# Kernel tuning notes

Hardware: AMD Instinct MI355X
Metric: run time of the kernel (lower is better)

The kernel has to match this reference:

```python
import jax, jax.numpy as jnp
import numpy as np


def setup_inputs() -> dict:
    key = jax.random.key(0)
    kx, ke = jax.random.split(key)
    N, T, D, M = 64, 400, 1024, 256
    x = jax.random.normal(kx, (N, T, D), dtype=jnp.float32)
    embedding = jax.random.normal(ke, (M, D), dtype=jnp.float32)
    return {"x": x, "embedding": embedding}


def reference(x, embedding):
    # x: (N, T, D); embedding (codebook): (M, D)
    M, D = embedding.shape
    # L2_distance: normalize codebook rows, distances to detached x
    emb_norm = embedding / (jnp.linalg.norm(embedding, axis=1, keepdims=True) + 1e-4)
    x_flat = jax.lax.stop_gradient(x).reshape(-1, D)  # (N*T, D)
    distances = (jnp.sum(emb_norm ** 2, axis=1)[None, :]
                 + jnp.sum(x_flat ** 2, axis=1, keepdims=True)
                 - 2.0 * (x_flat @ emb_norm.T))  # (N*T, M)
    indices = jnp.argmin(distances, axis=-1)  # (N*T,)
    encodings = jax.nn.one_hot(indices, M, dtype=jnp.float32)  # (N*T, M)
    quantized = embedding[indices].reshape(x.shape)  # gather from UNnormalized codebook

    # commitment loss (both sides detached in original -> constant)
    commitment_loss = jnp.mean(
        (jax.lax.stop_gradient(x) - jax.lax.stop_gradient(quantized)) ** 2)

    # straight-through + average with quantized
    quantized_st = x + jax.lax.stop_gradient(quantized - x)
    quantized_ = (quantized_st + quantized) / 2.0

    avg_probs = jnp.mean(encodings, axis=0)  # (M,)
    perplexity = jnp.exp(-jnp.sum(avg_probs * jnp.log(avg_probs + 1e-10)))
    return quantized_, commitment_loss, perplexity
```

## Files before the change

kernel.cpp:

```cpp
#include <hip/hip_runtime.h>
#include <cstdint>
#include <cstddef>


typedef __attribute__((ext_vector_type(8))) short short8;
typedef __attribute__((ext_vector_type(4))) float f32x4;

namespace {
constexpr int kNT = 25600;
constexpr int kD  = 1024;
constexpr int kM  = 256;
constexpr size_t kQElems = (size_t)kNT * kD;

constexpr int WS_IMG_H = 0;
constexpr int WS_IMG_L = 131072;
constexpr int WS_E2N   = 262144;
constexpr int WS_SCL   = WS_E2N + kM;
constexpr int WS_E2R   = WS_SCL + kM;
constexpr int WS_COM   = WS_E2R + kM;
constexpr int WS_HIST  = WS_COM + 4;
constexpr int WS_ZERO_BYTES = (WS_HIST + kM - WS_COM) * 4;
}

typedef __attribute__((address_space(3))) unsigned int        lds_u32;
typedef const __attribute__((address_space(1))) unsigned int  glb_u32;
typedef const __attribute__((address_space(3))) char          lds_chc;

__device__ __forceinline__ void gl2lds16(const void* g, void* l) {
  __builtin_amdgcn_global_load_lds((glb_u32*)g, (lds_u32*)l, 16, 0, 0);
}

template <int OFF>
__device__ __forceinline__ short8 ldsr(lds_chc* p) {
  short8 r;
  asm volatile("ds_read_b128 %0, %1 offset:%c2" : "=v"(r) : "v"(p), "i"(OFF));
  return r;
}

__global__ __launch_bounds__(256) void vq_normalize(const float* __restrict__ emb,
                                                    float* __restrict__ ws) {
  const int m = blockIdx.x;
  const int t = threadIdx.x;
  const float4 v = reinterpret_cast<const float4*>(emb + (size_t)m * kD)[t];
  float s = v.x * v.x + v.y * v.y + v.z * v.z + v.w * v.w;
#pragma unroll
  for (int mask = 32; mask >= 1; mask >>= 1) s += __shfl_xor(s, mask);
  __shared__ float red[4];
  if ((t & 63) == 0) red[t >> 6] = s;
  __syncthreads();
  const float tot = red[0] + red[1] + red[2] + red[3];
  const float sc  = sqrtf(tot) + 1e-4f;
  const float inv = 1.0f / sc;
  const float4 nv = make_float4(v.x * inv, v.y * inv, v.z * inv, v.w * inv);

  float s2 = nv.x * nv.x + nv.y * nv.y + nv.z * nv.z + nv.w * nv.w;
#pragma unroll
  for (int mask = 32; mask >= 1; mask >>= 1) s2 += __shfl_xor(s2, mask);
  __syncthreads();
  if ((t & 63) == 0) red[t >> 6] = s2;
  __syncthreads();
  if (t == 0) {
    ws[WS_E2N + m] = red[0] + red[1] + red[2] + red[3];
    ws[WS_SCL + m] = sc;
    ws[WS_E2R + m] = tot;
  }

  unsigned short* imgh = (unsigned short*)(ws + WS_IMG_H);
  unsigned short* imgl = (unsigned short*)(ws + WS_IMG_L);
  const int c  = t >> 3;
  const int g  = (t >> 1) & 3;
  const int sq = g ^ ((m >> 1) & 3);
  const int base = c * 8192 + m * 32 + sq * 8 + 4 * (t & 1);
  ushort4 hq, lq;
#pragma unroll
  for (int j = 0; j < 4; ++j) {
    const float fv = (&nv.x)[j];
    const unsigned int b = __float_as_uint(fv);
    const unsigned short hi = (unsigned short)(b >> 16);
    const float lof = fv - __uint_as_float(b & 0xFFFF0000u);
    const unsigned short lo = (unsigned short)(__float_as_uint(lof) >> 16);
    (&hq.x)[j] = hi; (&lq.x)[j] = lo;
  }
  *(ushort4*)(imgh + base) = hq;
  *(ushort4*)(imgl + base) = lq;
}


#define RD8(BSEL, G, H0, H1, H2, H3, L0, L1, L2, L3)                           \
  H0 = ldsr<(BSEL) * 32768 + ((G) * 4 + 0) * 1024>(lbase);                     \
  H1 = ldsr<(BSEL) * 32768 + ((G) * 4 + 1) * 1024>(lbase);                     \
  H2 = ldsr<(BSEL) * 32768 + ((G) * 4 + 2) * 1024>(lbase);                     \
  H3 = ldsr<(BSEL) * 32768 + ((G) * 4 + 3) * 1024>(lbase);                     \
  L0 = ldsr<(BSEL) * 32768 + 16384 + ((G) * 4 + 0) * 1024>(lbase);             \
  L1 = ldsr<(BSEL) * 32768 + 16384 + ((G) * 4 + 1) * 1024>(lbase);             \
  L2 = ldsr<(BSEL) * 32768 + 16384 + ((G) * 4 + 2) * 1024>(lbase);             \
  L3 = ldsr<(BSEL) * 32768 + 16384 + ((G) * 4 + 3) * 1024>(lbase);

#define MM12(G, H0, H1, H2, H3, L0, L1, L2, L3)                                              \
  acc[(G) * 4 + 0] = __builtin_amdgcn_mfma_f32_16x16x32_bf16(ah, H0, acc[(G) * 4 + 0], 0, 0, 0); \
  acc[(G) * 4 + 1] = __builtin_amdgcn_mfma_f32_16x16x32_bf16(ah, H1, acc[(G) * 4 + 1], 0, 0, 0); \
  acc[(G) * 4 + 2] = __builtin_amdgcn_mfma_f32_16x16x32_bf16(ah, H2, acc[(G) * 4 + 2], 0, 0, 0); \
  acc[(G) * 4 + 3] = __builtin_amdgcn_mfma_f32_16x16x32_bf16(ah, H3, acc[(G) * 4 + 3], 0, 0, 0); \
  acc[(G) * 4 + 0] = __builtin_amdgcn_mfma_f32_16x16x32_bf16(ah, L0, acc[(G) * 4 + 0], 0, 0, 0); \
  acc[(G) * 4 + 1] = __builtin_amdgcn_mfma_f32_16x16x32_bf16(ah, L1, acc[(G) * 4 + 1], 0, 0, 0); \
  acc[(G) * 4 + 2] = __builtin_amdgcn_mfma_f32_16x16x32_bf16(ah, L2, acc[(G) * 4 + 2], 0, 0, 0); \
  acc[(G) * 4 + 3] = __builtin_amdgcn_mfma_f32_16x16x32_bf16(ah, L3, acc[(G) * 4 + 3], 0, 0, 0); \
  acc[(G) * 4 + 0] = __builtin_amdgcn_mfma_f32_16x16x32_bf16(al, H0, acc[(G) * 4 + 0], 0, 0, 0); \
  acc[(G) * 4 + 1] = __builtin_amdgcn_mfma_f32_16x16x32_bf16(al, H1, acc[(G) * 4 + 1], 0, 0, 0); \
  acc[(G) * 4 + 2] = __builtin_amdgcn_mfma_f32_16x16x32_bf16(al, H2, acc[(G) * 4 + 2], 0, 0, 0); \
  acc[(G) * 4 + 3] = __builtin_amdgcn_mfma_f32_16x16x32_bf16(al, H3, acc[(G) * 4 + 3], 0, 0, 0);

#define VQ_ITER(KC, BSEL, XC0, XC1, XN0, XN1)                                  \
  {                                                                            \
    const int kcn_ = ((KC) < 31) ? (KC) + 1 : 31;                              \
    const float* xp_ = xrow + kcn_ * 32;                                       \
    XN0 = *(const float4*)xp_;                                                 \
    XN1 = *(const float4*)(xp_ + 4);                                           \
    {                                                                          \
      const unsigned short* sg_ = simg + ((size_t)kcn_ << 13) + soff;          \
      char* dg_ = &buf[(BSEL) ^ 1][0] + ldst;                                  \
      _Pragma("unroll")                                                        \
      for (int it_ = 0; it_ < 8; ++it_)                                        \
        gl2lds16(sg_ + it_ * 512, dg_ + it_ * 1024);                           \
    }                                                                          \
    asm volatile("s_waitcnt vmcnt(10)" ::: "memory");                          \
    __builtin_amdgcn_s_barrier();                                              \
    asm volatile("" ::: "memory");                                             \
    short8 ha0_, ha1_, ha2_, ha3_, la0_, la1_, la2_, la3_;                     \
    short8 hb0_, hb1_, hb2_, hb3_, lb0_, lb1_, lb2_, lb3_;                     \
    RD8((BSEL), 0, ha0_, ha1_, ha2_, ha3_, la0_, la1_, la2_, la3_)             \
    RD8((BSEL), 1, hb0_, hb1_, hb2_, hb3_, lb0_, lb1_, lb2_, lb3_)             \
    short8 ah, al;                                                             \
    {                                                                          \
      union { short8 v; unsigned short u[8]; } H_, L_;                         \
      const float fx_[8] = {XC0.x, XC0.y, XC0.z, XC0.w,                        \
                            XC1.x, XC1.y, XC1.z, XC1.w};                       \
      _Pragma("unroll")                                                        \
      for (int jj_ = 0; jj_ < 8; ++jj_) {                                      \
        const float fv_ = fx_[jj_];                                            \
        const unsigned int b_ = __float_as_uint(fv_);                          \
        H_.u[jj_] = (unsigned short)(b_ >> 16);                                \
        const float lo_ = fv_ - __uint_as_float(b_ & 0xFFFF0000u);             \
        L_.u[jj_] = (unsigned short)(__float_as_uint(lo_) >> 16);              \
        x2 += fv_ * fv_;                                                       \
      }                                                                        \
      ah = H_.v; al = L_.v;                                                    \
    }                                                                          \
    asm volatile("s_waitcnt lgkmcnt(8)" ::: "memory");                         \
    __builtin_amdgcn_sched_barrier(0);                                         \
    MM12(0, ha0_, ha1_, ha2_, ha3_, la0_, la1_, la2_, la3_)                    \
    RD8((BSEL), 2, ha0_, ha1_, ha2_, ha3_, la0_, la1_, la2_, la3_)             \
    asm volatile("s_waitcnt lgkmcnt(8)" ::: "memory");                         \
    __builtin_amdgcn_sched_barrier(0);                                         \
    MM12(1, hb0_, hb1_, hb2_, hb3_, lb0_, lb1_, lb2_, lb3_)                    \
    RD8((BSEL), 3, hb0_, hb1_, hb2_, hb3_, lb0_, lb1_, lb2_, lb3_)             \
    asm volatile("s_waitcnt lgkmcnt(8)" ::: "memory");                         \
    __builtin_amdgcn_sched_barrier(0);                                         \
    MM12(2, ha0_, ha1_, ha2_, ha3_, la0_, la1_, la2_, la3_)                    \
    asm volatile("s_waitcnt lgkmcnt(0)" ::: "memory");                         \
    __builtin_amdgcn_sched_barrier(0);                                         \
    MM12(3, hb0_, hb1_, hb2_, hb3_, lb0_, lb1_, lb2_, lb3_)                    \
    asm volatile("" ::: "memory");                                             \
    __builtin_amdgcn_s_barrier();                                              \
    asm volatile("" ::: "memory");                                             \
  }

__global__ __launch_bounds__(256, 2) void vq_main(const float* __restrict__ x,
                                                  const float* __restrict__ emb,
                                                  const float* __restrict__ wsc,
                                                  float* __restrict__ out,
                                                  float* __restrict__ commit_sum,
                                                  int* __restrict__ hist) {
  __shared__ char buf[2][32768];

  const int t   = threadIdx.x;
  const int l   = t & 63;
  const int w   = t >> 6;
  const int r0  = blockIdx.x * 64 + w * 16;
  const int nlo = l & 15;
  const int q   = l >> 4;
  const int sq  = q ^ ((l >> 1) & 3);

  const unsigned short* imgH = (const unsigned short*)(wsc + WS_IMG_H);
  const unsigned short* imgL = (const unsigned short*)(wsc + WS_IMG_L);
  const unsigned short* simg = (w & 2) ? imgL : imgH;
  const int soff = (w & 1) * 4096 + l * 8;
  const int ldst = w * 8192;

  const float* xrow = x + (size_t)(r0 + nlo) * kD + q * 8;
  lds_chc* lbase = (lds_chc*)&buf[0][0] + nlo * 64 + sq * 16;

  f32x4 acc[16];
#pragma unroll
  for (int i = 0; i < 16; ++i) acc[i] = (f32x4)0.0f;
  float x2 = 0.0f;

  float4 xa0, xa1, xb0, xb1;
  xa0 = *(const float4*)xrow;
  xa1 = *(const float4*)(xrow + 4);
  {
    const unsigned short* sg = simg + soff;
    char* dg = &buf[0][0] + ldst;
#pragma unroll
    for (int it = 0; it < 8; ++it) gl2lds16(sg + it * 512, dg + it * 1024);
  }

#pragma unroll 1
  for (int kk = 0; kk < 32; kk += 2) {
    VQ_ITER(kk,     0, xa0, xa1, xb0, xb1)
    VQ_ITER(kk + 1, 1, xb0, xb1, xa0, xa1)
  }

  x2 += __shfl_xor(x2, 16);
  x2 += __shfl_xor(x2, 32);

  float bv[4] = {3.0e38f, 3.0e38f, 3.0e38f, 3.0e38f};
  int   bj[4] = {0, 0, 0, 0};
#pragma unroll
  for (int ct = 0; ct < 16; ++ct) {
    const int j = ct * 16 + nlo;
    const float e = wsc[WS_E2N + j];
#pragma unroll
    for (int rg = 0; rg < 4; ++rg) {
      const float v = e - 2.0f * acc[ct][rg];
      if (v < bv[rg] || (v == bv[rg] && j < bj[rg])) { bv[rg] = v; bj[rg] = j; }
    }
  }
#pragma unroll
  for (int mk = 1; mk <= 8; mk <<= 1) {
#pragma unroll
    for (int rg = 0; rg < 4; ++rg) {
      const float ov = __shfl_xor(bv[rg], mk);
      const int   oj = __shfl_xor(bj[rg], mk);
      if (ov < bv[rg] || (ov == bv[rg] && oj < bj[rg])) { bv[rg] = ov; bj[rg] = oj; }
    }
  }

  float clq = 0.0f;
#pragma unroll
  for (int rg = 0; rg < 4; ++rg) {
    const int j = bj[rg];
    const float xr2 = __shfl(x2, (q << 2) | rg);
    clq += xr2 + wsc[WS_E2R + j] - (wsc[WS_E2N + j] - bv[rg]) * wsc[WS_SCL + j];
  }
  if (nlo == 0) {
#pragma unroll
    for (int rg = 0; rg < 4; ++rg) atomicAdd(&hist[bj[rg]], 1);
  }
  float cs = (nlo == 0) ? clq : 0.0f;
  cs += __shfl_xor(cs, 16);
  cs += __shfl_xor(cs, 32);
  if (l == 0) atomicAdd(commit_sum, cs);

  const float4* emb4 = (const float4*)emb;
  float4* out4 = (float4*)out;
#pragma unroll
  for (int r = 0; r < 16; ++r) {
    const int j = __shfl(bj[r & 3], (r >> 2) << 4);
    const float4* s = emb4 + (size_t)j * (kD / 4);
    float4* d = out4 + (size_t)(r0 + r) * (kD / 4);
#pragma unroll
    for (int c = 0; c < 4; ++c) d[c * 64 + l] = s[c * 64 + l];
  }
}

__global__ __launch_bounds__(256) void vq_final(const int* __restrict__ hist,
                                                const float* __restrict__ commit_sum,
                                                float* __restrict__ out) {
  const int t = threadIdx.x;
  const float p = (float)hist[t] * (1.0f / (float)kNT);
  float s = p * logf(p + 1e-10f);
#pragma unroll
  for (int mask = 32; mask >= 1; mask >>= 1) s += __shfl_xor(s, mask);
  __shared__ float red[4];
  if ((t & 63) == 0) red[t >> 6] = s;
  __syncthreads();
  if (t == 0) {
    const float ent = red[0] + red[1] + red[2] + red[3];
    out[kQElems]     = commit_sum[0] * (1.0f / (float)kQElems);
    out[kQElems + 1] = expf(-ent);
  }
}

extern "C" void kernel_launch(void* const* d_in, const int* in_sizes, int n_in,
                              void* d_out, int out_size, void* d_ws, size_t ws_size,
                              hipStream_t stream) {
  (void)in_sizes; (void)n_in; (void)out_size; (void)ws_size;
  const float* x   = (const float*)d_in[0];
  const float* emb = (const float*)d_in[1];
  float* out = (float*)d_out;
  float* ws  = (float*)d_ws;

  hipMemsetAsync((char*)d_ws + (size_t)WS_COM * 4, 0, WS_ZERO_BYTES, stream);
  hipLaunchKernelGGL(vq_normalize, dim3(kM), dim3(256), 0, stream, emb, ws);
  hipLaunchKernelGGL(vq_main, dim3(kNT / 64), dim3(256), 0, stream,
                     x, emb, ws, out, ws + WS_COM, (int*)(ws + WS_HIST));
  hipLaunchKernelGGL(vq_final, dim3(1), dim3(256), 0, stream,
                     (const int*)(ws + WS_HIST), ws + WS_COM, out);
}
```

Before: 252.6 us.

## Switch to 32x32x16 MFMA tiles with 128 rows per block

Replaces the 16x16x32 bf16 MFMA with 32x32x16 MFMA, so each wave now covers 32 rows instead of 16 and each block covers 128 rows. Every codebook tile staged in LDS is therefore reused across twice as many x rows, halving codebook traffic per row and the number of blocks. The argmin reduction and commitment-loss bookkeeping are reworked for the new accumulator layout, and the codebook norm arrays are cached in shared memory. In exchange, accumulator register use doubles, launch bounds drop to one block per CU, and there are only 200 blocks, which may underfill the GPU's CUs.

```diff
diff --git a/kernel.cpp b/kernel.cpp
--- a/kernel.cpp
+++ b/kernel.cpp
@@ -3,8 +3,8 @@
 #include <cstddef>
 
 
-typedef __attribute__((ext_vector_type(8))) short short8;
-typedef __attribute__((ext_vector_type(4))) float f32x4;
+typedef __attribute__((ext_vector_type(8)))  short short8;
+typedef __attribute__((ext_vector_type(16))) float f32x16;
 
 namespace {
 constexpr int kNT = 25600;
@@ -86,100 +86,110 @@
 }
 
 
-#define RD8(BSEL, G, H0, H1, H2, H3, L0, L1, L2, L3)                           \
-  H0 = ldsr<(BSEL) * 32768 + ((G) * 4 + 0) * 1024>(lbase);                     \
-  H1 = ldsr<(BSEL) * 32768 + ((G) * 4 + 1) * 1024>(lbase);                     \
-  H2 = ldsr<(BSEL) * 32768 + ((G) * 4 + 2) * 1024>(lbase);                     \
-  H3 = ldsr<(BSEL) * 32768 + ((G) * 4 + 3) * 1024>(lbase);                     \
-  L0 = ldsr<(BSEL) * 32768 + 16384 + ((G) * 4 + 0) * 1024>(lbase);             \
-  L1 = ldsr<(BSEL) * 32768 + 16384 + ((G) * 4 + 1) * 1024>(lbase);             \
-  L2 = ldsr<(BSEL) * 32768 + 16384 + ((G) * 4 + 2) * 1024>(lbase);             \
-  L3 = ldsr<(BSEL) * 32768 + 16384 + ((G) * 4 + 3) * 1024>(lbase);
-
-#define MM12(G, H0, H1, H2, H3, L0, L1, L2, L3)                                              \
-  acc[(G) * 4 + 0] = __builtin_amdgcn_mfma_f32_16x16x32_bf16(ah, H0, acc[(G) * 4 + 0], 0, 0, 0); \
-  acc[(G) * 4 + 1] = __builtin_amdgcn_mfma_f32_16x16x32_bf16(ah, H1, acc[(G) * 4 + 1], 0, 0, 0); \
-  acc[(G) * 4 + 2] = __builtin_amdgcn_mfma_f32_16x16x32_bf16(ah, H2, acc[(G) * 4 + 2], 0, 0, 0); \
-  acc[(G) * 4 + 3] = __builtin_amdgcn_mfma_f32_16x16x32_bf16(ah, H3, acc[(G) * 4 + 3], 0, 0, 0); \
-  acc[(G) * 4 + 0] = __builtin_amdgcn_mfma_f32_16x16x32_bf16(ah, L0, acc[(G) * 4 + 0], 0, 0, 0); \
-  acc[(G) * 4 + 1] = __builtin_amdgcn_mfma_f32_16x16x32_bf16(ah, L1, acc[(G) * 4 + 1], 0, 0, 0); \
-  acc[(G) * 4 + 2] = __builtin_amdgcn_mfma_f32_16x16x32_bf16(ah, L2, acc[(G) * 4 + 2], 0, 0, 0); \
-  acc[(G) * 4 + 3] = __builtin_amdgcn_mfma_f32_16x16x32_bf16(ah, L3, acc[(G) * 4 + 3], 0, 0, 0); \
-  acc[(G) * 4 + 0] = __builtin_amdgcn_mfma_f32_16x16x32_bf16(al, H0, acc[(G) * 4 + 0], 0, 0, 0); \
-  acc[(G) * 4 + 1] = __builtin_amdgcn_mfma_f32_16x16x32_bf16(al, H1, acc[(G) * 4 + 1], 0, 0, 0); \
-  acc[(G) * 4 + 2] = __builtin_amdgcn_mfma_f32_16x16x32_bf16(al, H2, acc[(G) * 4 + 2], 0, 0, 0); \
-  acc[(G) * 4 + 3] = __builtin_amdgcn_mfma_f32_16x16x32_bf16(al, H3, acc[(G) * 4 + 3], 0, 0, 0);
-
-#define VQ_ITER(KC, BSEL, XC0, XC1, XN0, XN1)                                  \
+#define RD8T(BSEL, T0, LB, H0, H1, H2, H3, L0, L1, L2, L3)                     \
+  H0 = ldsr<(BSEL) * 32768 + ((T0) + 0) * 2048>(LB);                           \
+  H1 = ldsr<(BSEL) * 32768 + ((T0) + 1) * 2048>(LB);                           \
+  H2 = ldsr<(BSEL) * 32768 + ((T0) + 2) * 2048>(LB);                           \
+  H3 = ldsr<(BSEL) * 32768 + ((T0) + 3) * 2048>(LB);                           \
+  L0 = ldsr<(BSEL) * 32768 + 16384 + ((T0) + 0) * 2048>(LB);                   \
+  L1 = ldsr<(BSEL) * 32768 + 16384 + ((T0) + 1) * 2048>(LB);                   \
+  L2 = ldsr<(BSEL) * 32768 + 16384 + ((T0) + 2) * 2048>(LB);                   \
+  L3 = ldsr<(BSEL) * 32768 + 16384 + ((T0) + 3) * 2048>(LB);
+
+#define MM12T(T0, AH, AL, H0, H1, H2, H3, L0, L1, L2, L3)                                          \
+  acc[(T0) + 0] = __builtin_amdgcn_mfma_f32_32x32x16_bf16(AH, H0, acc[(T0) + 0], 0, 0, 0);         \
+  acc[(T0) + 1] = __builtin_amdgcn_mfma_f32_32x32x16_bf16(AH, H1, acc[(T0) + 1], 0, 0, 0);         \
+  acc[(T0) + 2] = __builtin_amdgcn_mfma_f32_32x32x16_bf16(AH, H2, acc[(T0) + 2], 0, 0, 0);         \
+  acc[(T0) + 3] = __builtin_amdgcn_mfma_f32_32x32x16_bf16(AH, H3, acc[(T0) + 3], 0, 0, 0);         \
+  acc[(T0) + 0] = __builtin_amdgcn_mfma_f32_32x32x16_bf16(AH, L0, acc[(T0) + 0], 0, 0, 0);         \
+  acc[(T0) + 1] = __builtin_amdgcn_mfma_f32_32x32x16_bf16(AH, L1, acc[(T0) + 1], 0, 0, 0);         \
+  acc[(T0) + 2] = __builtin_amdgcn_mfma_f32_32x32x16_bf16(AH, L2, acc[(T0) + 2], 0, 0, 0);         \
+  acc[(T0) + 3] = __builtin_amdgcn_mfma_f32_32x32x16_bf16(AH, L3, acc[(T0) + 3], 0, 0, 0);         \
+  acc[(T0) + 0] = __builtin_amdgcn_mfma_f32_32x32x16_bf16(AL, H0, acc[(T0) + 0], 0, 0, 0);         \
+  acc[(T0) + 1] = __builtin_amdgcn_mfma_f32_32x32x16_bf16(AL, H1, acc[(T0) + 1], 0, 0, 0);         \
+  acc[(T0) + 2] = __builtin_amdgcn_mfma_f32_32x32x16_bf16(AL, H2, acc[(T0) + 2], 0, 0, 0);         \
+  acc[(T0) + 3] = __builtin_amdgcn_mfma_f32_32x32x16_bf16(AL, H3, acc[(T0) + 3], 0, 0, 0);
+
+#define CONV8(F0, F1, AH, AL)                                                  \
   {                                                                            \
+    union { short8 v; unsigned short u[8]; } H_, L_;                           \
+    const float fx_[8] = {F0.x, F0.y, F0.z, F0.w, F1.x, F1.y, F1.z, F1.w};     \
+    _Pragma("unroll")                                                          \
+    for (int jj_ = 0; jj_ < 8; ++jj_) {                                        \
+      const float fv_ = fx_[jj_];                                              \
+      const unsigned int b_ = __float_as_uint(fv_);                            \
+      H_.u[jj_] = (unsigned short)(b_ >> 16);                                  \
+      const float lo_ = fv_ - __uint_as_float(b_ & 0xFFFF0000u);               \
+      L_.u[jj_] = (unsigned short)(__float_as_uint(lo_) >> 16);                \
+      x2 += fv_ * fv_;                                                         \
+    }                                                                          \
+    AH = H_.v; AL = L_.v;                                                      \
+  }
+
+#define VQ_ITER3(KC, BSEL)                                                     \
+  {                                                                            \
+    short8 ah0, al0, ah1, al1;                                                 \
+    CONV8(xc0, xc1, ah0, al0)                      \
+    CONV8(xc2, xc3, ah1, al1)                      \
     const int kcn_ = ((KC) < 31) ? (KC) + 1 : 31;                              \
-    const float* xp_ = xrow + kcn_ * 32;                                       \
-    XN0 = *(const float4*)xp_;                                                 \
-    XN1 = *(const float4*)(xp_ + 4);                                           \
     {                                                                          \
+      const float* xp_ = xrow + kcn_ * 32;                                     \
+      xc0 = *(const float4*)(xp_);                                             \
+      xc1 = *(const float4*)(xp_ + 4);                                         \
+      xc2 = *(const float4*)(xp_ + 16);                                        \
+      xc3 = *(const float4*)(xp_ + 20);                                        \
       const unsigned short* sg_ = simg + ((size_t)kcn_ << 13) + soff;          \
       char* dg_ = &buf[(BSEL) ^ 1][0] + ldst;                                  \
       _Pragma("unroll")                                                        \
       for (int it_ = 0; it_ < 8; ++it_)                                        \
         gl2lds16(sg_ + it_ * 512, dg_ + it_ * 1024);                           \
     }                                                                          \
-    asm volatile("s_waitcnt vmcnt(10)" ::: "memory");                          \
+    asm volatile("s_waitcnt vmcnt(12)" ::: "memory");                          \
     __builtin_amdgcn_s_barrier();                                              \
     asm volatile("" ::: "memory");                                             \
-    short8 ha0_, ha1_, ha2_, ha3_, la0_, la1_, la2_, la3_;                     \
-    short8 hb0_, hb1_, hb2_, hb3_, lb0_, lb1_, lb2_, lb3_;                     \
-    RD8((BSEL), 0, ha0_, ha1_, ha2_, ha3_, la0_, la1_, la2_, la3_)             \
-    RD8((BSEL), 1, hb0_, hb1_, hb2_, hb3_, lb0_, lb1_, lb2_, lb3_)             \
-    short8 ah, al;                                                             \
-    {                                                                          \
-      union { short8 v; unsigned short u[8]; } H_, L_;                         \
-      const float fx_[8] = {XC0.x, XC0.y, XC0.z, XC0.w,                        \
-                            XC1.x, XC1.y, XC1.z, XC1.w};                       \
-      _Pragma("unroll")                                                        \
-      for (int jj_ = 0; jj_ < 8; ++jj_) {                                      \
-        const float fv_ = fx_[jj_];                                            \
-        const unsigned int b_ = __float_as_uint(fv_);                          \
-        H_.u[jj_] = (unsigned short)(b_ >> 16);                                \
-        const float lo_ = fv_ - __uint_as_float(b_ & 0xFFFF0000u);             \
-        L_.u[jj_] = (unsigned short)(__float_as_uint(lo_) >> 16);              \
-        x2 += fv_ * fv_;                                                       \
-      }                                                                        \
-      ah = H_.v; al = L_.v;                                                    \
-    }                                                                          \
+    short8 h0_, h1_, h2_, h3_, l0_, l1_, l2_, l3_;                             \
+    short8 h4_, h5_, h6_, h7_, l4_, l5_, l6_, l7_;                             \
+    RD8T((BSEL), 0, lb0, h0_, h1_, h2_, h3_, l0_, l1_, l2_, l3_)               \
+    RD8T((BSEL), 4, lb0, h4_, h5_, h6_, h7_, l4_, l5_, l6_, l7_)               \
     asm volatile("s_waitcnt lgkmcnt(8)" ::: "memory");                         \
     __builtin_amdgcn_sched_barrier(0);                                         \
-    MM12(0, ha0_, ha1_, ha2_, ha3_, la0_, la1_, la2_, la3_)                    \
-    RD8((BSEL), 2, ha0_, ha1_, ha2_, ha3_, la0_, la1_, la2_, la3_)             \
+    MM12T(0, ah0, al0, h0_, h1_, h2_, h3_, l0_, l1_, l2_, l3_)                 \
+    RD8T((BSEL), 0, lb1, h0_, h1_, h2_, h3_, l0_, l1_, l2_, l3_)               \
     asm volatile("s_waitcnt lgkmcnt(8)" ::: "memory");                         \
     __builtin_amdgcn_sched_barrier(0);                                         \
-    MM12(1, hb0_, hb1_, hb2_, hb3_, lb0_, lb1_, lb2_, lb3_)                    \
-    RD8((BSEL), 3, hb0_, hb1_, hb2_, hb3_, lb0_, lb1_, lb2_, lb3_)             \
+    MM12T(4, ah0, al0, h4_, h5_, h6_, h7_, l4_, l5_, l6_, l7_)                 \
+    RD8T((BSEL), 4, lb1, h4_, h5_, h6_, h7_, l4_, l5_, l6_, l7_)               \
     asm volatile("s_waitcnt lgkmcnt(8)" ::: "memory");                         \
     __builtin_amdgcn_sched_barrier(0);                                         \
-    MM12(2, ha0_, ha1_, ha2_, ha3_, la0_, la1_, la2_, la3_)                    \
+    MM12T(0, ah1, al1, h0_, h1_, h2_, h3_, l0_, l1_, l2_, l3_)                 \
     asm volatile("s_waitcnt lgkmcnt(0)" ::: "memory");                         \
     __builtin_amdgcn_sched_barrier(0);                                         \
-    MM12(3, hb0_, hb1_, hb2_, hb3_, lb0_, lb1_, lb2_, lb3_)                    \
+    MM12T(4, ah1, al1, h4_, h5_, h6_, h7_, l4_, l5_, l6_, l7_)                 \
     asm volatile("" ::: "memory");                                             \
     __builtin_amdgcn_s_barrier();                                              \
     asm volatile("" ::: "memory");                                             \
   }
 
-__global__ __launch_bounds__(256, 2) void vq_main(const float* __restrict__ x,
+__global__ __launch_bounds__(256, 1) void vq_main(const float* __restrict__ x,
                                                   const float* __restrict__ emb,
                                                   const float* __restrict__ wsc,
                                                   float* __restrict__ out,
                                                   float* __restrict__ commit_sum,
                                                   int* __restrict__ hist) {
   __shared__ char buf[2][32768];
+  __shared__ float e2n_s[kM], scl_s[kM], e2r_s[kM];
 
   const int t   = threadIdx.x;
   const int l   = t & 63;
   const int w   = t >> 6;
-  const int r0  = blockIdx.x * 64 + w * 16;
-  const int nlo = l & 15;
-  const int q   = l >> 4;
-  const int sq  = q ^ ((l >> 1) & 3);
+  const int n32 = l & 31;
+  const int hw  = l >> 5;
+  const int r0w = blockIdx.x * 128 + w * 32;
+  const int row = r0w + n32;
+
+  e2n_s[t] = wsc[WS_E2N + t];
+  scl_s[t] = wsc[WS_SCL + t];
+  e2r_s[t] = wsc[WS_E2R + t];
 
   const unsigned short* imgH = (const unsigned short*)(wsc + WS_IMG_H);
   const unsigned short* imgL = (const unsigned short*)(wsc + WS_IMG_L);
@@ -187,17 +197,23 @@
   const int soff = (w & 1) * 4096 + l * 8;
   const int ldst = w * 8192;
 
-  const float* xrow = x + (size_t)(r0 + nlo) * kD + q * 8;
-  lds_chc* lbase = (lds_chc*)&buf[0][0] + nlo * 64 + sq * 16;
-
-  f32x4 acc[16];
-#pragma unroll
-  for (int i = 0; i < 16; ++i) acc[i] = (f32x4)0.0f;
+  const float* xrow = x + (size_t)row * kD + hw * 8;
+
+  const int q3  = (n32 >> 1) & 3;
+  const int sq0 = hw ^ q3;
+  const int sq1 = (2 + hw) ^ q3;
+  lds_chc* lb0 = (lds_chc*)&buf[0][0] + n32 * 64 + sq0 * 16;
+  lds_chc* lb1 = (lds_chc*)&buf[0][0] + n32 * 64 + sq1 * 16;
+
+  f32x16 acc[8];
+#pragma unroll
+  for (int i = 0; i < 8; ++i) acc[i] = (f32x16)0.0f;
   float x2 = 0.0f;
 
-  float4 xa0, xa1, xb0, xb1;
-  xa0 = *(const float4*)xrow;
-  xa1 = *(const float4*)(xrow + 4);
+  float4 xc0 = *(const float4*)(xrow);
+  float4 xc1 = *(const float4*)(xrow + 4);
+  float4 xc2 = *(const float4*)(xrow + 16);
+  float4 xc3 = *(const float4*)(xrow + 20);
   {
     const unsigned short* sg = simg + soff;
     char* dg = &buf[0][0] + ldst;
@@ -207,58 +223,59 @@
 
 #pragma unroll 1
   for (int kk = 0; kk < 32; kk += 2) {
-    VQ_ITER(kk,     0, xa0, xa1, xb0, xb1)
-    VQ_ITER(kk + 1, 1, xb0, xb1, xa0, xa1)
-  }
-
-  x2 += __shfl_xor(x2, 16);
+    VQ_ITER3(kk, 0)
+    VQ_ITER3(kk + 1, 1)
+  }
+
   x2 += __shfl_xor(x2, 32);
 
-  float bv[4] = {3.0e38f, 3.0e38f, 3.0e38f, 3.0e38f};
-  int   bj[4] = {0, 0, 0, 0};
-#pragma unroll
-  for (int ct = 0; ct < 16; ++ct) {
-    const int j = ct * 16 + nlo;
-    const float e = wsc[WS_E2N + j];
-#pragma unroll
-    for (int rg = 0; rg < 4; ++rg) {
+  float bv[16]; int bj[16];
+#pragma unroll
+  for (int i = 0; i < 16; ++i) { bv[i] = 3.0e38f; bj[i] = 0; }
+#pragma unroll
+  for (int ct = 0; ct < 8; ++ct) {
+    const int j = ct * 32 + n32;
+    const float e = e2n_s[j];
+#pragma unroll
+    for (int rg = 0; rg < 16; ++rg) {
       const float v = e - 2.0f * acc[ct][rg];
       if (v < bv[rg] || (v == bv[rg] && j < bj[rg])) { bv[rg] = v; bj[rg] = j; }
     }
   }
 #pragma unroll
-  for (int mk = 1; mk <= 8; mk <<= 1) {
-#pragma unroll
-    for (int rg = 0; rg < 4; ++rg) {
+  for (int mk = 1; mk <= 16; mk <<= 1) {
+#pragma unroll
+    for (int rg = 0; rg < 16; ++rg) {
       const float ov = __shfl_xor(bv[rg], mk);
       const int   oj = __shfl_xor(bj[rg], mk);
       if (ov < bv[rg] || (ov == bv[rg] && oj < bj[rg])) { bv[rg] = ov; bj[rg] = oj; }
     }
   }
-
-  float clq = 0.0f;
-#pragma unroll
-  for (int rg = 0; rg < 4; ++rg) {
-    const int j = bj[rg];
-    const float xr2 = __shfl(x2, (q << 2) | rg);
-    clq += xr2 + wsc[WS_E2R + j] - (wsc[WS_E2N + j] - bv[rg]) * wsc[WS_SCL + j];
-  }
-  if (nlo == 0) {
-#pragma unroll
-    for (int rg = 0; rg < 4; ++rg) atomicAdd(&hist[bj[rg]], 1);
-  }
-  float cs = (nlo == 0) ? clq : 0.0f;
-  cs += __shfl_xor(cs, 16);
-  cs += __shfl_xor(cs, 32);
-  if (l == 0) atomicAdd(commit_sum, cs);
+  const int regr  = (n32 & 3) | ((n32 >> 3) << 2);
+  const int hwant = (n32 >> 2) & 1;
+  float bvr = bv[0]; int bjr = bj[0];
+#pragma unroll
+  for (int rg = 1; rg < 16; ++rg)
+    if (regr == rg) { bvr = bv[rg]; bjr = bj[rg]; }
+  {
+    const float ov = __shfl_xor(bvr, 32);
+    const int   oj = __shfl_xor(bjr, 32);
+    if (hwant != hw) { bvr = ov; bjr = oj; }
+  }
+
+  float cl = x2 + e2r_s[bjr] - (e2n_s[bjr] - bvr) * scl_s[bjr];
+#pragma unroll
+  for (int mk = 1; mk <= 32; mk <<= 1) cl += __shfl_xor(cl, mk);
+  if (l == 0) atomicAdd(commit_sum, cl * 0.5f);
+  if (hw == 0) atomicAdd(&hist[bjr], 1);
 
   const float4* emb4 = (const float4*)emb;
   float4* out4 = (float4*)out;
-#pragma unroll
-  for (int r = 0; r < 16; ++r) {
-    const int j = __shfl(bj[r & 3], (r >> 2) << 4);
+#pragma unroll 2
+  for (int r = 0; r < 32; ++r) {
+    const int j = __shfl(bjr, r);
     const float4* s = emb4 + (size_t)j * (kD / 4);
-    float4* d = out4 + (size_t)(r0 + r) * (kD / 4);
+    float4* d = out4 + (size_t)(r0w + r) * (kD / 4);
 #pragma unroll
     for (int c = 0; c < 4; ++c) d[c * 64 + l] = s[c * 64 + l];
   }
@@ -293,7 +310,7 @@
 
   hipMemsetAsync((char*)d_ws + (size_t)WS_COM * 4, 0, WS_ZERO_BYTES, stream);
   hipLaunchKernelGGL(vq_normalize, dim3(kM), dim3(256), 0, stream, emb, ws);
-  hipLaunchKernelGGL(vq_main, dim3(kNT / 64), dim3(256), 0, stream,
+  hipLaunchKernelGGL(vq_main, dim3(kNT / 128), dim3(256), 0, stream,
                      x, emb, ws, out, ws + WS_COM, (int*)(ws + WS_HIST));
   hipLaunchKernelGGL(vq_final, dim3(1), dim3(256), 0, stream,
                      (const int*)(ws + WS_HIST), ws + WS_COM, out);
```

New measurement: 255.8 us. Within noise of the previous version (+1.3%).

## Restructure VQ main kernel into 256 persistent 14-wave blocks with codebook split

Applied to the files above, without the earlier changes.

Launches 256 blocks of 896 threads (14 waves), each covering 100 rows, with waves split across row tiles and two codebook halves. Only 8 waves stage the codebook image, into a triple-buffered LDS ring. The per-iteration trailing barrier is gone, and MFMA sections raise wave priority via setprio. Partial argmins from the two halves are merged through shared memory, and the norm tables are cached in LDS. The aim is more codebook reuse per staged tile and better load/compute overlap. The cost is more block-level syncs, padded rows in the last block, and lower occupancy from one block per CU.

```diff
diff --git a/kernel.cpp b/kernel.cpp
--- a/kernel.cpp
+++ b/kernel.cpp
@@ -86,130 +86,166 @@
 }
 
 
-#define RD8(BSEL, G, H0, H1, H2, H3, L0, L1, L2, L3)                           \
-  H0 = ldsr<(BSEL) * 32768 + ((G) * 4 + 0) * 1024>(lbase);                     \
-  H1 = ldsr<(BSEL) * 32768 + ((G) * 4 + 1) * 1024>(lbase);                     \
-  H2 = ldsr<(BSEL) * 32768 + ((G) * 4 + 2) * 1024>(lbase);                     \
-  H3 = ldsr<(BSEL) * 32768 + ((G) * 4 + 3) * 1024>(lbase);                     \
-  L0 = ldsr<(BSEL) * 32768 + 16384 + ((G) * 4 + 0) * 1024>(lbase);             \
-  L1 = ldsr<(BSEL) * 32768 + 16384 + ((G) * 4 + 1) * 1024>(lbase);             \
-  L2 = ldsr<(BSEL) * 32768 + 16384 + ((G) * 4 + 2) * 1024>(lbase);             \
-  L3 = ldsr<(BSEL) * 32768 + 16384 + ((G) * 4 + 3) * 1024>(lbase);
-
-#define MM12(G, H0, H1, H2, H3, L0, L1, L2, L3)                                              \
-  acc[(G) * 4 + 0] = __builtin_amdgcn_mfma_f32_16x16x32_bf16(ah, H0, acc[(G) * 4 + 0], 0, 0, 0); \
-  acc[(G) * 4 + 1] = __builtin_amdgcn_mfma_f32_16x16x32_bf16(ah, H1, acc[(G) * 4 + 1], 0, 0, 0); \
-  acc[(G) * 4 + 2] = __builtin_amdgcn_mfma_f32_16x16x32_bf16(ah, H2, acc[(G) * 4 + 2], 0, 0, 0); \
-  acc[(G) * 4 + 3] = __builtin_amdgcn_mfma_f32_16x16x32_bf16(ah, H3, acc[(G) * 4 + 3], 0, 0, 0); \
-  acc[(G) * 4 + 0] = __builtin_amdgcn_mfma_f32_16x16x32_bf16(ah, L0, acc[(G) * 4 + 0], 0, 0, 0); \
-  acc[(G) * 4 + 1] = __builtin_amdgcn_mfma_f32_16x16x32_bf16(ah, L1, acc[(G) * 4 + 1], 0, 0, 0); \
-  acc[(G) * 4 + 2] = __builtin_amdgcn_mfma_f32_16x16x32_bf16(ah, L2, acc[(G) * 4 + 2], 0, 0, 0); \
-  acc[(G) * 4 + 3] = __builtin_amdgcn_mfma_f32_16x16x32_bf16(ah, L3, acc[(G) * 4 + 3], 0, 0, 0); \
-  acc[(G) * 4 + 0] = __builtin_amdgcn_mfma_f32_16x16x32_bf16(al, H0, acc[(G) * 4 + 0], 0, 0, 0); \
-  acc[(G) * 4 + 1] = __builtin_amdgcn_mfma_f32_16x16x32_bf16(al, H1, acc[(G) * 4 + 1], 0, 0, 0); \
-  acc[(G) * 4 + 2] = __builtin_amdgcn_mfma_f32_16x16x32_bf16(al, H2, acc[(G) * 4 + 2], 0, 0, 0); \
-  acc[(G) * 4 + 3] = __builtin_amdgcn_mfma_f32_16x16x32_bf16(al, H3, acc[(G) * 4 + 3], 0, 0, 0);
-
-#define VQ_ITER(KC, BSEL, XC0, XC1, XN0, XN1)                                  \
+#define RD8(LB, T0, H0, H1, H2, H3, L0, L1, L2, L3)                            \
+  H0 = ldsr<((T0) + 0) * 1024>(LB);                                            \
+  H1 = ldsr<((T0) + 1) * 1024>(LB);                                            \
+  H2 = ldsr<((T0) + 2) * 1024>(LB);                                            \
+  H3 = ldsr<((T0) + 3) * 1024>(LB);                                            \
+  L0 = ldsr<16384 + ((T0) + 0) * 1024>(LB);                                    \
+  L1 = ldsr<16384 + ((T0) + 1) * 1024>(LB);                                    \
+  L2 = ldsr<16384 + ((T0) + 2) * 1024>(LB);                                    \
+  L3 = ldsr<16384 + ((T0) + 3) * 1024>(LB);
+
+#define MM12(T0, H0, H1, H2, H3, L0, L1, L2, L3)                                                 \
+  acc[(T0) + 0] = __builtin_amdgcn_mfma_f32_16x16x32_bf16(ah, H0, acc[(T0) + 0], 0, 0, 0);       \
+  acc[(T0) + 1] = __builtin_amdgcn_mfma_f32_16x16x32_bf16(ah, H1, acc[(T0) + 1], 0, 0, 0);       \
+  acc[(T0) + 2] = __builtin_amdgcn_mfma_f32_16x16x32_bf16(ah, H2, acc[(T0) + 2], 0, 0, 0);       \
+  acc[(T0) + 3] = __builtin_amdgcn_mfma_f32_16x16x32_bf16(ah, H3, acc[(T0) + 3], 0, 0, 0);       \
+  acc[(T0) + 0] = __builtin_amdgcn_mfma_f32_16x16x32_bf16(ah, L0, acc[(T0) + 0], 0, 0, 0);       \
+  acc[(T0) + 1] = __builtin_amdgcn_mfma_f32_16x16x32_bf16(ah, L1, acc[(T0) + 1], 0, 0, 0);       \
+  acc[(T0) + 2] = __builtin_amdgcn_mfma_f32_16x16x32_bf16(ah, L2, acc[(T0) + 2], 0, 0, 0);       \
+  acc[(T0) + 3] = __builtin_amdgcn_mfma_f32_16x16x32_bf16(ah, L3, acc[(T0) + 3], 0, 0, 0);       \
+  acc[(T0) + 0] = __builtin_amdgcn_mfma_f32_16x16x32_bf16(al, H0, acc[(T0) + 0], 0, 0, 0);       \
+  acc[(T0) + 1] = __builtin_amdgcn_mfma_f32_16x16x32_bf16(al, H1, acc[(T0) + 1], 0, 0, 0);       \
+  acc[(T0) + 2] = __builtin_amdgcn_mfma_f32_16x16x32_bf16(al, H2, acc[(T0) + 2], 0, 0, 0);       \
+  acc[(T0) + 3] = __builtin_amdgcn_mfma_f32_16x16x32_bf16(al, L3 , acc[(T0) + 3], 0, 0, 0);
+
+#undef MM12
+#define MM12(T0, H0, H1, H2, H3, L0, L1, L2, L3)                                                 \
+  acc[(T0) + 0] = __builtin_amdgcn_mfma_f32_16x16x32_bf16(ah, H0, acc[(T0) + 0], 0, 0, 0);       \
+  acc[(T0) + 1] = __builtin_amdgcn_mfma_f32_16x16x32_bf16(ah, H1, acc[(T0) + 1], 0, 0, 0);       \
+  acc[(T0) + 2] = __builtin_amdgcn_mfma_f32_16x16x32_bf16(ah, H2, acc[(T0) + 2], 0, 0, 0);       \
+  acc[(T0) + 3] = __builtin_amdgcn_mfma_f32_16x16x32_bf16(ah, H3, acc[(T0) + 3], 0, 0, 0);       \
+  acc[(T0) + 0] = __builtin_amdgcn_mfma_f32_16x16x32_bf16(ah, L0, acc[(T0) + 0], 0, 0, 0);       \
+  acc[(T0) + 1] = __builtin_amdgcn_mfma_f32_16x16x32_bf16(ah, L1, acc[(T0) + 1], 0, 0, 0);       \
+  acc[(T0) + 2] = __builtin_amdgcn_mfma_f32_16x16x32_bf16(ah, L2, acc[(T0) + 2], 0, 0, 0);       \
+  acc[(T0) + 3] = __builtin_amdgcn_mfma_f32_16x16x32_bf16(ah, L3, acc[(T0) + 3], 0, 0, 0);       \
+  acc[(T0) + 0] = __builtin_amdgcn_mfma_f32_16x16x32_bf16(al, H0, acc[(T0) + 0], 0, 0, 0);       \
+  acc[(T0) + 1] = __builtin_amdgcn_mfma_f32_16x16x32_bf16(al, H1, acc[(T0) + 1], 0, 0, 0);       \
+  acc[(T0) + 2] = __builtin_amdgcn_mfma_f32_16x16x32_bf16(al, H2, acc[(T0) + 2], 0, 0, 0);       \
+  acc[(T0) + 3] = __builtin_amdgcn_mfma_f32_16x16x32_bf16(al, H3, acc[(T0) + 3], 0, 0, 0);
+
+#define CONV8(F0, F1)                                                          \
+  {                                                                            \
+    union { short8 v; unsigned short u[8]; } H_, L_;                           \
+    const float fx_[8] = {F0.x, F0.y, F0.z, F0.w, F1.x, F1.y, F1.z, F1.w};     \
+    _Pragma("unroll")                                                          \
+    for (int jj_ = 0; jj_ < 8; ++jj_) {                                        \
+      const float fv_ = fx_[jj_];                                              \
+      const unsigned int b_ = __float_as_uint(fv_);                            \
+      H_.u[jj_] = (unsigned short)(b_ >> 16);                                  \
+      const float lo_ = fv_ - __uint_as_float(b_ & 0xFFFF0000u);               \
+      L_.u[jj_] = (unsigned short)(__float_as_uint(lo_) >> 16);                \
+      x2 += fv_ * fv_;                                                         \
+    }                                                                          \
+    ah = H_.v; al = L_.v;                                                      \
+  }
+
+#define VQ_ITER4(KC, RB, SB, XC0, XC1, XN0, XN1)                               \
   {                                                                            \
     const int kcn_ = ((KC) < 31) ? (KC) + 1 : 31;                              \
     const float* xp_ = xrow + kcn_ * 32;                                       \
     XN0 = *(const float4*)xp_;                                                 \
     XN1 = *(const float4*)(xp_ + 4);                                           \
-    {                                                                          \
+    if (stg) {                                                                 \
       const unsigned short* sg_ = simg + ((size_t)kcn_ << 13) + soff;          \
-      char* dg_ = &buf[(BSEL) ^ 1][0] + ldst;                                  \
+      char* dg_ = &buf[SB][0] + ldst;                                          \
       _Pragma("unroll")                                                        \
-      for (int it_ = 0; it_ < 8; ++it_)                                        \
+      for (int it_ = 0; it_ < 4; ++it_)                                        \
         gl2lds16(sg_ + it_ * 512, dg_ + it_ * 1024);                           \
+      asm volatile("s_waitcnt vmcnt(6)" ::: "memory");                         \
+    } else {                                                                   \
+      asm volatile("s_waitcnt vmcnt(2)" ::: "memory");                         \
     }                                                                          \
-    asm volatile("s_waitcnt vmcnt(10)" ::: "memory");                          \
     __builtin_amdgcn_s_barrier();                                              \
     asm volatile("" ::: "memory");                                             \
-    short8 ha0_, ha1_, ha2_, ha3_, la0_, la1_, la2_, la3_;                     \
-    short8 hb0_, hb1_, hb2_, hb3_, lb0_, lb1_, lb2_, lb3_;                     \
-    RD8((BSEL), 0, ha0_, ha1_, ha2_, ha3_, la0_, la1_, la2_, la3_)             \
-    RD8((BSEL), 1, hb0_, hb1_, hb2_, hb3_, lb0_, lb1_, lb2_, lb3_)             \
+    lds_chc* lb_ = lbase + (RB) * 32768;                                       \
+    short8 h0_, h1_, h2_, h3_, l0_, l1_, l2_, l3_;                             \
+    RD8(lb_, 0, h0_, h1_, h2_, h3_, l0_, l1_, l2_, l3_)                        \
     short8 ah, al;                                                             \
-    {                                                                          \
-      union { short8 v; unsigned short u[8]; } H_, L_;                         \
-      const float fx_[8] = {XC0.x, XC0.y, XC0.z, XC0.w,                        \
-                            XC1.x, XC1.y, XC1.z, XC1.w};                       \
-      _Pragma("unroll")                                                        \
-      for (int jj_ = 0; jj_ < 8; ++jj_) {                                      \
-        const float fv_ = fx_[jj_];                                            \
-        const unsigned int b_ = __float_as_uint(fv_);                          \
-        H_.u[jj_] = (unsigned short)(b_ >> 16);                                \
-        const float lo_ = fv_ - __uint_as_float(b_ & 0xFFFF0000u);             \
-        L_.u[jj_] = (unsigned short)(__float_as_uint(lo_) >> 16);              \
-        x2 += fv_ * fv_;                                                       \
-      }                                                                        \
-      ah = H_.v; al = L_.v;                                                    \
-    }                                                                          \
-    asm volatile("s_waitcnt lgkmcnt(8)" ::: "memory");                         \
-    __builtin_amdgcn_sched_barrier(0);                                         \
-    MM12(0, ha0_, ha1_, ha2_, ha3_, la0_, la1_, la2_, la3_)                    \
-    RD8((BSEL), 2, ha0_, ha1_, ha2_, ha3_, la0_, la1_, la2_, la3_)             \
-    asm volatile("s_waitcnt lgkmcnt(8)" ::: "memory");                         \
-    __builtin_amdgcn_sched_barrier(0);                                         \
-    MM12(1, hb0_, hb1_, hb2_, hb3_, lb0_, lb1_, lb2_, lb3_)                    \
-    RD8((BSEL), 3, hb0_, hb1_, hb2_, hb3_, lb0_, lb1_, lb2_, lb3_)             \
-    asm volatile("s_waitcnt lgkmcnt(8)" ::: "memory");                         \
-    __builtin_amdgcn_sched_barrier(0);                                         \
-    MM12(2, ha0_, ha1_, ha2_, ha3_, la0_, la1_, la2_, la3_)                    \
+    CONV8(XC0, XC1)                                                            \
     asm volatile("s_waitcnt lgkmcnt(0)" ::: "memory");                         \
     __builtin_amdgcn_sched_barrier(0);                                         \
-    MM12(3, hb0_, hb1_, hb2_, hb3_, lb0_, lb1_, lb2_, lb3_)                    \
-    asm volatile("" ::: "memory");                                             \
-    __builtin_amdgcn_s_barrier();                                              \
-    asm volatile("" ::: "memory");                                             \
-  }
-
-__global__ __launch_bounds__(256, 2) void vq_main(const float* __restrict__ x,
+    __builtin_amdgcn_s_setprio(1);                                             \
+    MM12(0, h0_, h1_, h2_, h3_, l0_, l1_, l2_, l3_)                            \
+    __builtin_amdgcn_s_setprio(0);                                             \
+    RD8(lb_, 4, h0_, h1_, h2_, h3_, l0_, l1_, l2_, l3_)                        \
+    asm volatile("s_waitcnt lgkmcnt(0)" ::: "memory");                         \
+    __builtin_amdgcn_sched_barrier(0);                                         \
+    __builtin_amdgcn_s_setprio(1);                                             \
+    MM12(4, h0_, h1_, h2_, h3_, l0_, l1_, l2_, l3_)                            \
+    __builtin_amdgcn_s_setprio(0);                                             \
+  }
+
+__global__ __launch_bounds__(896, 1) void vq_main(const float* __restrict__ x,
                                                   const float* __restrict__ emb,
                                                   const float* __restrict__ wsc,
                                                   float* __restrict__ out,
                                                   float* __restrict__ commit_sum,
                                                   int* __restrict__ hist) {
-  __shared__ char buf[2][32768];
+  __shared__ char buf[3][32768];
+  __shared__ float e2n_s[kM], scl_s[kM], e2r_s[kM];
+  __shared__ float bvp[7][2][16];
+  __shared__ int   bjp[7][2][16];
+  __shared__ int   idx_s[112];
 
   const int t   = threadIdx.x;
   const int l   = t & 63;
   const int w   = t >> 6;
-  const int r0  = blockIdx.x * 64 + w * 16;
+  const int rt  = w >> 1;
+  const int ch  = w & 1;
   const int nlo = l & 15;
-  const int q   = l >> 4;
-  const int sq  = q ^ ((l >> 1) & 3);
-
+  const int kq  = l >> 4;
+  const int blk0 = blockIdx.x * 100;
+  const int lrow = rt * 16 + nlo;
+  const int growc = (blk0 + lrow < kNT) ? (blk0 + lrow) : (kNT - 1);
+  const float* xrow = x + (size_t)growc * kD + kq * 8;
+
+  if (t < kM) {
+    e2n_s[t] = wsc[WS_E2N + t];
+    scl_s[t] = wsc[WS_SCL + t];
+    e2r_s[t] = wsc[WS_E2R + t];
+  }
+
+  const bool stg = (w < 8);
   const unsigned short* imgH = (const unsigned short*)(wsc + WS_IMG_H);
   const unsigned short* imgL = (const unsigned short*)(wsc + WS_IMG_L);
-  const unsigned short* simg = (w & 2) ? imgL : imgH;
-  const int soff = (w & 1) * 4096 + l * 8;
-  const int ldst = w * 8192;
-
-  const float* xrow = x + (size_t)(r0 + nlo) * kD + q * 8;
-  lds_chc* lbase = (lds_chc*)&buf[0][0] + nlo * 64 + sq * 16;
-
-  f32x4 acc[16];
-#pragma unroll
-  for (int i = 0; i < 16; ++i) acc[i] = (f32x4)0.0f;
+  const unsigned short* simg = (w < 4) ? imgH : imgL;
+  const int part = w & 3;
+  const int soff = part * 2048 + l * 8;
+  const int ldst = ((w < 4) ? 0 : 16384) + part * 4096;
+
+  const int sq = kq ^ ((nlo >> 1) & 3);
+  lds_chc* lbase = (lds_chc*)&buf[0][0] + ch * 8192 + nlo * 64 + sq * 16;
+
+  f32x4 acc[8];
+#pragma unroll
+  for (int i = 0; i < 8; ++i) acc[i] = (f32x4)0.0f;
   float x2 = 0.0f;
 
-  float4 xa0, xa1, xb0, xb1;
-  xa0 = *(const float4*)xrow;
-  xa1 = *(const float4*)(xrow + 4);
-  {
+  __syncthreads();
+
+  float4 xa0 = *(const float4*)xrow;
+  float4 xa1 = *(const float4*)(xrow + 4);
+  float4 xb0, xb1;
+  if (stg) {
     const unsigned short* sg = simg + soff;
     char* dg = &buf[0][0] + ldst;
 #pragma unroll
-    for (int it = 0; it < 8; ++it) gl2lds16(sg + it * 512, dg + it * 1024);
+    for (int it = 0; it < 4; ++it) gl2lds16(sg + it * 512, dg + it * 1024);
   }
 
 #pragma unroll 1
-  for (int kk = 0; kk < 32; kk += 2) {
-    VQ_ITER(kk,     0, xa0, xa1, xb0, xb1)
-    VQ_ITER(kk + 1, 1, xb0, xb1, xa0, xa1)
-  }
+  for (int kk = 0; kk < 30; kk += 6) {
+    VQ_ITER4(kk,     0, 1, xa0, xa1, xb0, xb1)
+    VQ_ITER4(kk + 1, 1, 2, xb0, xb1, xa0, xa1)
+    VQ_ITER4(kk + 2, 2, 0, xa0, xa1, xb0, xb1)
+    VQ_ITER4(kk + 3, 0, 1, xb0, xb1, xa0, xa1)
+    VQ_ITER4(kk + 4, 1, 2, xa0, xa1, xb0, xb1)
+    VQ_ITER4(kk + 5, 2, 0, xb0, xb1, xa0, xa1)
+  }
+  VQ_ITER4(30, 0, 1, xa0, xa1, xb0, xb1)
+  VQ_ITER4(31, 1, 2, xb0, xb1, xa0, xa1)
 
   x2 += __shfl_xor(x2, 16);
   x2 += __shfl_xor(x2, 32);
@@ -217,9 +253,9 @@
   float bv[4] = {3.0e38f, 3.0e38f, 3.0e38f, 3.0e38f};
   int   bj[4] = {0, 0, 0, 0};
 #pragma unroll
-  for (int ct = 0; ct < 16; ++ct) {
-    const int j = ct * 16 + nlo;
-    const float e = wsc[WS_E2N + j];
+  for (int ct = 0; ct < 8; ++ct) {
+    const int j = ch * 128 + ct * 16 + nlo;
+    const float e = e2n_s[j];
 #pragma unroll
     for (int rg = 0; rg < 4; ++rg) {
       const float v = e - 2.0f * acc[ct][rg];
@@ -235,32 +271,51 @@
       if (ov < bv[rg] || (ov == bv[rg] && oj < bj[rg])) { bv[rg] = ov; bj[rg] = oj; }
     }
   }
-
-  float clq = 0.0f;
-#pragma unroll
-  for (int rg = 0; rg < 4; ++rg) {
-    const int j = bj[rg];
-    const float xr2 = __shfl(x2, (q << 2) | rg);
-    clq += xr2 + wsc[WS_E2R + j] - (wsc[WS_E2N + j] - bv[rg]) * wsc[WS_SCL + j];
-  }
   if (nlo == 0) {
 #pragma unroll
-    for (int rg = 0; rg < 4; ++rg) atomicAdd(&hist[bj[rg]], 1);
-  }
-  float cs = (nlo == 0) ? clq : 0.0f;
-  cs += __shfl_xor(cs, 16);
-  cs += __shfl_xor(cs, 32);
-  if (l == 0) atomicAdd(commit_sum, cs);
+    for (int rg = 0; rg < 4; ++rg) {
+      bvp[rt][ch][kq * 4 + rg] = bv[rg];
+      bjp[rt][ch][kq * 4 + rg] = bj[rg];
+    }
+  }
+  __syncthreads();
+
+  if (ch == 0) {
+    float clq = 0.0f;
+#pragma unroll
+    for (int rg = 0; rg < 4; ++rg) {
+      const int r = kq * 4 + rg;
+      float v0 = bvp[rt][0][r]; int j0 = bjp[rt][0][r];
+      const float v1 = bvp[rt][1][r]; const int j1 = bjp[rt][1][r];
+      if (v1 < v0 || (v1 == v0 && j1 < j0)) { v0 = v1; j0 = j1; }
+      const float xr2 = __shfl(x2, r);
+      const bool valid = (rt * 16 + r) < 100;
+      if (nlo == 0) {
+        idx_s[rt * 16 + r] = j0;
+        if (valid) atomicAdd(&hist[j0], 1);
+      }
+      if (valid)
+        clq += xr2 + e2r_s[j0] - (e2n_s[j0] - v0) * scl_s[j0];
+    }
+    float cs = (nlo == 0) ? clq : 0.0f;
+#pragma unroll
+    for (int mk = 1; mk <= 32; mk <<= 1) cs += __shfl_xor(cs, mk);
+    if (l == 0) atomicAdd(commit_sum, cs);
+  }
+  __syncthreads();
 
   const float4* emb4 = (const float4*)emb;
   float4* out4 = (float4*)out;
 #pragma unroll
-  for (int r = 0; r < 16; ++r) {
-    const int j = __shfl(bj[r & 3], (r >> 2) << 4);
-    const float4* s = emb4 + (size_t)j * (kD / 4);
-    float4* d = out4 + (size_t)(r0 + r) * (kD / 4);
-#pragma unroll
-    for (int c = 0; c < 4; ++c) d[c * 64 + l] = s[c * 64 + l];
+  for (int rr = 0; rr < 8; ++rr) {
+    const int lr = w * 8 + rr;
+    if (lr < 100) {
+      const int j = idx_s[lr];
+      const float4* s = emb4 + (size_t)j * (kD / 4);
+      float4* d = out4 + (size_t)(blk0 + lr) * (kD / 4);
+#pragma unroll
+      for (int c = 0; c < 4; ++c) d[c * 64 + l] = s[c * 64 + l];
+    }
   }
 }
 
@@ -293,7 +348,7 @@
 
   hipMemsetAsync((char*)d_ws + (size_t)WS_COM * 4, 0, WS_ZERO_BYTES, stream);
   hipLaunchKernelGGL(vq_normalize, dim3(kM), dim3(256), 0, stream, emb, ws);
-  hipLaunchKernelGGL(vq_main, dim3(kNT / 64), dim3(256), 0, stream,
+  hipLaunchKernelGGL(vq_main, dim3(256), dim3(896), 0, stream,
                      x, emb, ws, out, ws + WS_COM, (int*)(ws + WS_HIST));
   hipLaunchKernelGGL(vq_final, dim3(1), dim3(256), 0, stream,
                      (const int*)(ws + WS_HIST), ws + WS_COM, out);
```

Measured after the change: 313.8 us. 1.24x slower.
